# Kernel tuning notes

Measured on AMD Instinct MI355X. Metric: run time of the kernel, lower is better.

Reference implementation:

```python
import jax, jax.numpy as jnp
import numpy as np

NUM_OUT_POINTS = 1024  # init kwarg num_out_points


def setup_inputs() -> dict:
    key = jax.random.key(0)
    x = jax.random.normal(key, (128, 3, 32768), dtype=jnp.float32)
    return {"x": x}


def _fps_indices(pts, k):
    """Furthest point sampling. pts: [B, N, 3] -> idx [B, k] int32.
    Matches the standard CUDA kernel: start at point 0, iteratively pick the
    point with max min-distance to the selected set."""
    B, N, _ = pts.shape
    idx0 = jnp.zeros((B,), jnp.int32)
    mindist0 = jnp.full((B, N), 1e10, pts.dtype)

    def step(carry, _):
        mindist, last = carry
        # coordinates of the most recently selected point: [B, 1, 3]
        p_last = jnp.take_along_axis(pts, last[:, None, None], axis=1)
        d = jnp.sum((pts - p_last) ** 2, axis=-1)          # [B, N]
        mindist = jnp.minimum(mindist, d)
        nxt = jnp.argmax(mindist, axis=-1).astype(jnp.int32)
        return (mindist, nxt), nxt

    (_, _), rest = jax.lax.scan(step, (mindist0, idx0), None, length=k - 1)
    # rest: [k-1, B]; prepend the initial index 0
    return jnp.concatenate([idx0[None, :], rest], axis=0).T  # [B, k]


def reference(x):
    # x: [B, 3, N]; permute=False so y = x
    pts = jnp.transpose(x, (0, 2, 1))                      # [B, N, 3]
    idx = _fps_indices(pts, NUM_OUT_POINTS)                # [B, k]
    y = jnp.take_along_axis(pts, idx[..., None], axis=1)   # [B, k, 3]
    return jnp.transpose(y, (0, 2, 1))                     # [B, 3, k]
```

## Files before the change

kernel.cpp:

```cpp
#include <hip/hip_runtime.h>

#define BATCH    128
#define NPTS     32768
#define KOUT     1024
#define NTHREADS 512
#define PPT      (NPTS / NTHREADS)

__global__ __launch_bounds__(NTHREADS)
void fps_kernel(const float* __restrict__ x, float* __restrict__ out) {
    __shared__ float s_md[NPTS];
    __shared__ float s_redv[8];
    __shared__ int   s_redi[8];
    __shared__ float s_pt[3];

    const int b   = blockIdx.x;
    const int tid = threadIdx.x;
    const float* __restrict__ xb = x + (size_t)b * 3 * NPTS;
    float* __restrict__ ob = out + (size_t)b * 3 * KOUT;

    float xs[PPT], ys[PPT], zs[PPT];
#pragma unroll
    for (int i = 0; i < PPT; ++i) {
        const int n = tid + i * NTHREADS;
        xs[i] = xb[n];
        ys[i] = xb[NPTS + n];
        zs[i] = xb[2 * NPTS + n];
        s_md[n] = 1e10f;
    }

    float px = xb[0], py = xb[NPTS], pz = xb[2 * NPTS];
    if (tid == 0) {
        ob[0] = px; ob[KOUT] = py; ob[2 * KOUT] = pz;
    }
    __syncthreads();

    const int lane = tid & 63;
    const int wave = tid >> 6;

    for (int j = 1; j < KOUT; ++j) {
        float best = -1.0f;
        int   bi   = 0x7fffffff;

#pragma unroll
        for (int i = 0; i < PPT; ++i) {
            const int n = tid + i * NTHREADS;
            const float dx = __fsub_rn(xs[i], px);
            const float dy = __fsub_rn(ys[i], py);
            const float dz = __fsub_rn(zs[i], pz);
            const float d  = __fmaf_rn(dz, dz,
                              __fmaf_rn(dy, dy,
                                __fmul_rn(dx, dx)));
            const float m  = fminf(s_md[n], d);
            s_md[n] = m;
            if (m > best) { best = m; bi = n; }
        }

#pragma unroll
        for (int s = 1; s < 64; s <<= 1) {
            const float ov = __shfl_xor(best, s, 64);
            const int   oi = __shfl_xor(bi,   s, 64);
            if (ov > best || (ov == best && oi < bi)) { best = ov; bi = oi; }
        }
        if (lane == 0) { s_redv[wave] = best; s_redi[wave] = bi; }
        __syncthreads();

        if (wave == 0) {
            float v  = (lane < 8) ? s_redv[lane] : -1.0f;
            int   vi = (lane < 8) ? s_redi[lane] : 0x7fffffff;
#pragma unroll
            for (int s = 1; s < 8; s <<= 1) {
                const float ov = __shfl_xor(v,  s, 64);
                const int   oi = __shfl_xor(vi, s, 64);
                if (ov > v || (ov == v && oi < vi)) { v = ov; vi = oi; }
            }
            if (lane == 0) {
                const float sx = xb[vi];
                const float sy = xb[NPTS + vi];
                const float sz = xb[2 * NPTS + vi];
                s_pt[0] = sx; s_pt[1] = sy; s_pt[2] = sz;
                ob[j] = sx; ob[KOUT + j] = sy; ob[2 * KOUT + j] = sz;
            }
        }
        __syncthreads();
        px = s_pt[0]; py = s_pt[1]; pz = s_pt[2];
    }
}

extern "C" void kernel_launch(void* const* d_in, const int* in_sizes, int n_in,
                              void* d_out, int out_size, void* d_ws, size_t ws_size,
                              hipStream_t stream) {
    const float* x = (const float*)d_in[0];
    float* out = (float*)d_out;
    fps_kernel<<<BATCH, NTHREADS, 0, stream>>>(x, out);
}
```

Measured before the change: 4.039 ms.

## Split each batch across two cooperating blocks with global-memory handshake for argmax

Each batch's point cloud is split between two workgroups, and the grid grows to 256 blocks. Each block handles half the points and keeps half the min-distance array in shared memory. Per iteration, the two partners exchange a packed (distance, index) key through a workspace slot using release/acquire atomics and spin-wait, then both pick the global winner. This halves per-block work and uses more CUs, since 128 blocks underfill the device. In exchange, every one of the 1023 iterations pays a cross-CU global-memory synchronization latency, and the spin-wait deadlocks if the partner blocks are not co-resident.

```diff
diff --git a/kernel.cpp b/kernel.cpp
--- a/kernel.cpp
+++ b/kernel.cpp
@@ -2,34 +2,51 @@
 
 #define BATCH    128
 #define NPTS     32768
+#define HALFN    (NPTS / 2)
 #define KOUT     1024
 #define NTHREADS 512
-#define PPT      (NPTS / NTHREADS)
+#define PPT      (HALFN / NTHREADS)
+
+struct __align__(16) Slot {
+    unsigned long long key;
+    unsigned int       seq;
+};
+#define SLOT_STRIDE 128
+#define WS_NEEDED   (256 * SLOT_STRIDE)
 
 __global__ __launch_bounds__(NTHREADS)
-void fps_kernel(const float* __restrict__ x, float* __restrict__ out) {
-    __shared__ float s_md[NPTS];
+void fps_pair_kernel(const float* __restrict__ x, float* __restrict__ out,
+                     char* __restrict__ ws) {
+    __shared__ float s_md[HALFN];
     __shared__ float s_redv[8];
     __shared__ int   s_redi[8];
     __shared__ float s_pt[3];
 
-    const int b   = blockIdx.x;
-    const int tid = threadIdx.x;
+    const int bid  = blockIdx.x;
+    const int b    = bid & (BATCH - 1);
+    const int half = bid >> 7;
+    const int tid  = threadIdx.x;
+    const int base = half * HALFN;
+
     const float* __restrict__ xb = x + (size_t)b * 3 * NPTS;
     float* __restrict__ ob = out + (size_t)b * 3 * KOUT;
+
+    Slot* myslot = (Slot*)(ws + (size_t)bid * SLOT_STRIDE);
+    Slot* paslot = (Slot*)(ws + (size_t)(bid ^ 128) * SLOT_STRIDE);
 
     float xs[PPT], ys[PPT], zs[PPT];
 #pragma unroll
     for (int i = 0; i < PPT; ++i) {
-        const int n = tid + i * NTHREADS;
+        const int nl = tid + i * NTHREADS;
+        const int n  = base + nl;
         xs[i] = xb[n];
         ys[i] = xb[NPTS + n];
         zs[i] = xb[2 * NPTS + n];
-        s_md[n] = 1e10f;
+        s_md[nl] = 1e10f;
     }
 
     float px = xb[0], py = xb[NPTS], pz = xb[2 * NPTS];
-    if (tid == 0) {
+    if (half == 0 && tid == 0) {
         ob[0] = px; ob[KOUT] = py; ob[2 * KOUT] = pz;
     }
     __syncthreads();
@@ -43,16 +60,16 @@
 
 #pragma unroll
         for (int i = 0; i < PPT; ++i) {
-            const int n = tid + i * NTHREADS;
+            const int nl = tid + i * NTHREADS;
             const float dx = __fsub_rn(xs[i], px);
             const float dy = __fsub_rn(ys[i], py);
             const float dz = __fsub_rn(zs[i], pz);
             const float d  = __fmaf_rn(dz, dz,
                               __fmaf_rn(dy, dy,
                                 __fmul_rn(dx, dx)));
-            const float m  = fminf(s_md[n], d);
-            s_md[n] = m;
-            if (m > best) { best = m; bi = n; }
+            const float m  = fminf(s_md[nl], d);
+            s_md[nl] = m;
+            if (m > best) { best = m; bi = base + nl; }
         }
 
 #pragma unroll
@@ -74,9 +91,89 @@
                 if (ov > v || (ov == v && oi < vi)) { v = ov; vi = oi; }
             }
             if (lane == 0) {
-                const float sx = xb[vi];
-                const float sy = xb[NPTS + vi];
-                const float sz = xb[2 * NPTS + vi];
+                const unsigned long long key =
+                    ((unsigned long long)__float_as_uint(v) << 32) |
+                    (unsigned long long)(0xffffffffu - (unsigned)vi);
+                __hip_atomic_store(&myslot->key, key,
+                                   __ATOMIC_RELAXED, __HIP_MEMORY_SCOPE_AGENT);
+                __hip_atomic_store(&myslot->seq, (unsigned)j,
+                                   __ATOMIC_RELEASE, __HIP_MEMORY_SCOPE_AGENT);
+                while (__hip_atomic_load(&paslot->seq, __ATOMIC_ACQUIRE,
+                                         __HIP_MEMORY_SCOPE_AGENT) < (unsigned)j) {}
+                const unsigned long long pkey =
+                    __hip_atomic_load(&paslot->key,
+                                      __ATOMIC_RELAXED, __HIP_MEMORY_SCOPE_AGENT);
+                const unsigned long long wkey = (pkey > key) ? pkey : key;
+                const int widx = (int)(0xffffffffu - (unsigned)(wkey & 0xffffffffu));
+                const float sx = xb[widx];
+                const float sy = xb[NPTS + widx];
+                const float sz = xb[2 * NPTS + widx];
+                s_pt[0] = sx; s_pt[1] = sy; s_pt[2] = sz;
+                if (half == 0) {
+                    ob[j] = sx; ob[KOUT + j] = sy; ob[2 * KOUT + j] = sz;
+                }
+            }
+        }
+        __syncthreads();
+        px = s_pt[0]; py = s_pt[1]; pz = s_pt[2];
+    }
+}
+
+__global__ __launch_bounds__(NTHREADS)
+void fps_single_kernel(const float* __restrict__ x, float* __restrict__ out) {
+    __shared__ float s_md[NPTS];
+    __shared__ float s_redv[8];
+    __shared__ int   s_redi[8];
+    __shared__ float s_pt[3];
+
+    const int b   = blockIdx.x;
+    const int tid = threadIdx.x;
+    const float* __restrict__ xb = x + (size_t)b * 3 * NPTS;
+    float* __restrict__ ob = out + (size_t)b * 3 * KOUT;
+#define SPPT (NPTS / NTHREADS)
+    float xs[SPPT], ys[SPPT], zs[SPPT];
+#pragma unroll
+    for (int i = 0; i < SPPT; ++i) {
+        const int n = tid + i * NTHREADS;
+        xs[i] = xb[n]; ys[i] = xb[NPTS + n]; zs[i] = xb[2 * NPTS + n];
+        s_md[n] = 1e10f;
+    }
+    float px = xb[0], py = xb[NPTS], pz = xb[2 * NPTS];
+    if (tid == 0) { ob[0] = px; ob[KOUT] = py; ob[2 * KOUT] = pz; }
+    __syncthreads();
+    const int lane = tid & 63, wave = tid >> 6;
+    for (int j = 1; j < KOUT; ++j) {
+        float best = -1.0f; int bi = 0x7fffffff;
+#pragma unroll
+        for (int i = 0; i < SPPT; ++i) {
+            const int n = tid + i * NTHREADS;
+            const float dx = __fsub_rn(xs[i], px);
+            const float dy = __fsub_rn(ys[i], py);
+            const float dz = __fsub_rn(zs[i], pz);
+            const float d  = __fmaf_rn(dz, dz, __fmaf_rn(dy, dy, __fmul_rn(dx, dx)));
+            const float m  = fminf(s_md[n], d);
+            s_md[n] = m;
+            if (m > best) { best = m; bi = n; }
+        }
+#pragma unroll
+        for (int s = 1; s < 64; s <<= 1) {
+            const float ov = __shfl_xor(best, s, 64);
+            const int   oi = __shfl_xor(bi,   s, 64);
+            if (ov > best || (ov == best && oi < bi)) { best = ov; bi = oi; }
+        }
+        if (lane == 0) { s_redv[wave] = best; s_redi[wave] = bi; }
+        __syncthreads();
+        if (wave == 0) {
+            float v  = (lane < 8) ? s_redv[lane] : -1.0f;
+            int   vi = (lane < 8) ? s_redi[lane] : 0x7fffffff;
+#pragma unroll
+            for (int s = 1; s < 8; s <<= 1) {
+                const float ov = __shfl_xor(v,  s, 64);
+                const int   oi = __shfl_xor(vi, s, 64);
+                if (ov > v || (ov == v && oi < vi)) { v = ov; vi = oi; }
+            }
+            if (lane == 0) {
+                const float sx = xb[vi], sy = xb[NPTS + vi], sz = xb[2 * NPTS + vi];
                 s_pt[0] = sx; s_pt[1] = sy; s_pt[2] = sz;
                 ob[j] = sx; ob[KOUT + j] = sy; ob[2 * KOUT + j] = sz;
             }
@@ -91,5 +188,10 @@
                               hipStream_t stream) {
     const float* x = (const float*)d_in[0];
     float* out = (float*)d_out;
-    fps_kernel<<<BATCH, NTHREADS, 0, stream>>>(x, out);
+    if (ws_size >= WS_NEEDED) {
+        hipMemsetAsync(d_ws, 0, WS_NEEDED, stream);
+        fps_pair_kernel<<<2 * BATCH, NTHREADS, 0, stream>>>(x, out, (char*)d_ws);
+    } else {
+        fps_single_kernel<<<BATCH, NTHREADS, 0, stream>>>(x, out);
+    }
 }
```

Measured after the change: 6.247 ms. +54.7%, slower.
